# Kernel tuning notes

Hardware: AMD Instinct MI355X
Metric: run time of the kernel (lower is better)

## Reference

```python
import jax, jax.numpy as jnp
import numpy as np

BS, NQ, NH, HD = 4, 10000, 8, 32   # batch, queries, heads, head_dim
NP = 4                              # sampling points
H, W = 100, 100                     # fixed spatial shape (value_spatial_shapes_list[0])


def grid_sample_bilinear_zeros(img, grid):
    """PyTorch F.grid_sample(mode='bilinear', padding_mode='zeros', align_corners=False).
    img: (N, C, Hin, Win); grid: (N, Hg, Wg, 2) with (x, y) in [-1, 1].
    Returns (N, C, Hg, Wg)."""
    N, C, Hin, Win = img.shape
    Hg, Wg = grid.shape[1], grid.shape[2]
    # unnormalize (align_corners=False)
    x = (grid[..., 0] + 1.0) * (Win * 0.5) - 0.5
    y = (grid[..., 1] + 1.0) * (Hin * 0.5) - 0.5
    x0 = jnp.floor(x); y0 = jnp.floor(y)
    x1 = x0 + 1.0;     y1 = y0 + 1.0
    wx1 = x - x0; wx0 = 1.0 - wx1
    wy1 = y - y0; wy0 = 1.0 - wy1
    img_flat = img.reshape(N, C, Hin * Win)

    def gather(xi, yi, w):
        xi_i = xi.astype(jnp.int32); yi_i = yi.astype(jnp.int32)
        valid = (xi_i >= 0) & (xi_i < Win) & (yi_i >= 0) & (yi_i < Hin)
        xc = jnp.clip(xi_i, 0, Win - 1); yc = jnp.clip(yi_i, 0, Hin - 1)
        idx = (yc * Win + xc).reshape(N, 1, Hg * Wg)
        vals = jnp.take_along_axis(img_flat, idx, axis=2)      # (N, C, Hg*Wg)
        wm = jnp.where(valid, w, 0.0).reshape(N, 1, Hg * Wg)
        return vals * wm

    out = (gather(x0, y0, wx0 * wy0) + gather(x1, y0, wx1 * wy0)
           + gather(x0, y1, wx0 * wy1) + gather(x1, y1, wx1 * wy1))
    return out.reshape(N, C, Hg, Wg)


def setup_inputs() -> dict:
    key = jax.random.key(0)
    k1, k2, k3 = jax.random.split(key, 3)
    value = jax.random.normal(k1, (BS, H * W, NH, HD), dtype=jnp.float32)
    value_spatial_shapes = jnp.array([[H, W]], dtype=jnp.int64)  # unused (fixed-size variant)
    sampling_locations = jax.random.uniform(k2, (BS, NQ, NH, 1, NP, 2), dtype=jnp.float32)
    attention_weights = jax.random.uniform(k3, (BS, NQ, NH, 1, NP), dtype=jnp.float32)
    return {"value": value, "value_spatial_shapes": value_spatial_shapes,
            "sampling_locations": sampling_locations, "attention_weights": attention_weights}


def reference(value, value_spatial_shapes, sampling_locations, attention_weights):
    bs, _, nh, d = value.shape
    nq, npnt = sampling_locations.shape[1], sampling_locations.shape[4]
    # (bs, HW, nh, d) -> (bs*nh, d, H, W)
    v = jnp.transpose(value, (0, 2, 3, 1)).reshape(bs * nh, d, H, W)
    # sampling grids in [-1, 1]; single level -> index 0
    grids = 2.0 * sampling_locations[:, :, :, 0] - 1.0           # (bs, nq, nh, np, 2)
    grids = jnp.transpose(grids, (0, 2, 1, 3, 4)).reshape(bs * nh, nq, npnt, 2)
    sampled = grid_sample_bilinear_zeros(v, grids)               # (bs*nh, d, nq, np)
    aw = jnp.transpose(attention_weights, (0, 2, 1, 3, 4)).reshape(bs * nh, 1, nq, npnt)
    out = (sampled * aw).sum(-1)                                 # (bs*nh, d, nq)
    out = out.reshape(bs, nh * d, nq)
    return jnp.transpose(out, (0, 2, 1))                         # (bs, nq, nh*d)
```

## Files before the change

kernel.cpp:

```cpp
#include <hip/hip_runtime.h>


constexpr int BS = 4, NQ = 10000, NH = 8, HD = 32, NP = 4, H = 100, W = 100;
constexpr int HW = H * W;
constexpr int NGROUP = BS * NQ * NH;
constexpr int LANES_PER_GROUP = 8;

typedef float f32x4 __attribute__((ext_vector_type(4)));

__global__ __launch_bounds__(256)
void deform_attn_kernel(const float* __restrict__ value,
                        const float* __restrict__ sloc,
                        const float* __restrict__ aw,
                        float* __restrict__ out)
{
    const int tid   = blockIdx.x * 256 + threadIdx.x;
    const int group = tid >> 3;
    const int lane  = tid & 7;
    if (group >= NGROUP) return;

    const int h  = group & (NH - 1);
    const int bq = group >> 3;
    const int b  = bq / NQ;

    const f32x4 l01 = __builtin_nontemporal_load((const f32x4*)(sloc + (size_t)group * (NP * 2)));
    const f32x4 l23 = __builtin_nontemporal_load((const f32x4*)(sloc + (size_t)group * (NP * 2) + 4));
    const f32x4 wv  = __builtin_nontemporal_load((const f32x4*)(aw   + (size_t)group * NP));

    const float lx[NP] = {l01.x, l01.z, l23.x, l23.z};
    const float ly[NP] = {l01.y, l01.w, l23.y, l23.w};
    const float wp[NP] = {wv.x,  wv.y,  wv.z,  wv.w};

    const float* vbase = value + (size_t)b * HW * NH * HD + h * HD + lane * 4;

    f32x4 acc = (f32x4)(0.f);

#pragma unroll
    for (int p = 0; p < NP; ++p) {
        const float x = lx[p] * (float)W - 0.5f;
        const float y = ly[p] * (float)H - 0.5f;
        const float x0f = floorf(x);
        const float y0f = floorf(y);
        const int   x0  = (int)x0f, y0 = (int)y0f;
        const int   x1  = x0 + 1,   y1 = y0 + 1;
        const float wx1 = x - x0f,  wx0 = 1.f - wx1;
        const float wy1 = y - y0f,  wy0 = 1.f - wy1;

        const bool vx0 = (unsigned)x0 < (unsigned)W;
        const bool vx1 = (unsigned)x1 < (unsigned)W;
        const bool vy0 = (unsigned)y0 < (unsigned)H;
        const bool vy1 = (unsigned)y1 < (unsigned)H;

        const int xc0 = min(max(x0, 0), W - 1);
        const int xc1 = min(max(x1, 0), W - 1);
        const int yc0 = min(max(y0, 0), H - 1);
        const int yc1 = min(max(y1, 0), H - 1);

        const float w00 = (vx0 && vy0) ? wp[p] * wx0 * wy0 : 0.f;
        const float w10 = (vx1 && vy0) ? wp[p] * wx1 * wy0 : 0.f;
        const float w01 = (vx0 && vy1) ? wp[p] * wx0 * wy1 : 0.f;
        const float w11 = (vx1 && vy1) ? wp[p] * wx1 * wy1 : 0.f;

        const f32x4 v00 = *(const f32x4*)(vbase + (size_t)(yc0 * W + xc0) * (NH * HD));
        const f32x4 v10 = *(const f32x4*)(vbase + (size_t)(yc0 * W + xc1) * (NH * HD));
        const f32x4 v01 = *(const f32x4*)(vbase + (size_t)(yc1 * W + xc0) * (NH * HD));
        const f32x4 v11 = *(const f32x4*)(vbase + (size_t)(yc1 * W + xc1) * (NH * HD));

        acc += w00 * v00 + w10 * v10 + w01 * v01 + w11 * v11;
    }

    __builtin_nontemporal_store(acc, (f32x4*)(out + (size_t)bq * (NH * HD) + h * HD + lane * 4));
}

extern "C" void kernel_launch(void* const* d_in, const int* in_sizes, int n_in,
                              void* d_out, int out_size, void* d_ws, size_t ws_size,
                              hipStream_t stream) {
    const float* value = (const float*)d_in[0];
    const float* sloc  = (const float*)d_in[2];
    const float* aw    = (const float*)d_in[3];
    float*       out   = (float*)d_out;

    const int total_threads = NGROUP * LANES_PER_GROUP;
    const int block = 256;
    const int grid  = (total_threads + block - 1) / block;
    deform_attn_kernel<<<grid, block, 0, stream>>>(value, sloc, aw, out);
}
```

Before: 151.6 us.

## Remap blocks by batch/head-half and process two queries per thread

```diff
diff --git a/kernel.cpp b/kernel.cpp
--- a/kernel.cpp
+++ b/kernel.cpp
@@ -3,38 +3,15 @@
 
 constexpr int BS = 4, NQ = 10000, NH = 8, HD = 32, NP = 4, H = 100, W = 100;
 constexpr int HW = H * W;
-constexpr int NGROUP = BS * NQ * NH;
-constexpr int LANES_PER_GROUP = 8;
+constexpr int NQH = NQ / 2;
 
 typedef float f32x4 __attribute__((ext_vector_type(4)));
 
-__global__ __launch_bounds__(256)
-void deform_attn_kernel(const float* __restrict__ value,
-                        const float* __restrict__ sloc,
-                        const float* __restrict__ aw,
-                        float* __restrict__ out)
+__device__ __forceinline__ void bilinear_accum(const float lx[NP], const float ly[NP],
+                                               const float wp[NP],
+                                               const float* __restrict__ vbase,
+                                               f32x4& acc)
 {
-    const int tid   = blockIdx.x * 256 + threadIdx.x;
-    const int group = tid >> 3;
-    const int lane  = tid & 7;
-    if (group >= NGROUP) return;
-
-    const int h  = group & (NH - 1);
-    const int bq = group >> 3;
-    const int b  = bq / NQ;
-
-    const f32x4 l01 = __builtin_nontemporal_load((const f32x4*)(sloc + (size_t)group * (NP * 2)));
-    const f32x4 l23 = __builtin_nontemporal_load((const f32x4*)(sloc + (size_t)group * (NP * 2) + 4));
-    const f32x4 wv  = __builtin_nontemporal_load((const f32x4*)(aw   + (size_t)group * NP));
-
-    const float lx[NP] = {l01.x, l01.z, l23.x, l23.z};
-    const float ly[NP] = {l01.y, l01.w, l23.y, l23.w};
-    const float wp[NP] = {wv.x,  wv.y,  wv.z,  wv.w};
-
-    const float* vbase = value + (size_t)b * HW * NH * HD + h * HD + lane * 4;
-
-    f32x4 acc = (f32x4)(0.f);
-
 #pragma unroll
     for (int p = 0; p < NP; ++p) {
         const float x = lx[p] * (float)W - 0.5f;
@@ -68,8 +45,54 @@
 
         acc += w00 * v00 + w10 * v10 + w01 * v01 + w11 * v11;
     }
+}
 
-    __builtin_nontemporal_store(acc, (f32x4*)(out + (size_t)bq * (NH * HD) + h * HD + lane * 4));
+__global__ __launch_bounds__(256)
+void deform_attn_kernel(const float* __restrict__ value,
+                        const float* __restrict__ sloc,
+                        const float* __restrict__ aw,
+                        float* __restrict__ out)
+{
+    const int quad = blockIdx.x & 7;
+    const int c    = blockIdx.x >> 3;
+
+    const int t    = threadIdx.x;
+    const int lane = t & 7;
+    const int h_i  = (t >> 3) & 3;
+    const int slot = t >> 5;
+
+    const int b = quad >> 1;
+    const int h = ((quad & 1) << 2) + h_i;
+    const int q = (c << 3) + slot;
+
+    const int bq1 = b * NQ + q;
+    const int bq2 = bq1 + NQH;
+
+    const size_t p1 = (size_t)bq1 * NH + h;
+    const size_t p2 = (size_t)bq2 * NH + h;
+    const f32x4 a01 = *(const f32x4*)(sloc + p1 * (NP * 2));
+    const f32x4 a23 = *(const f32x4*)(sloc + p1 * (NP * 2) + 4);
+    const f32x4 awa = *(const f32x4*)(aw   + p1 * NP);
+    const f32x4 b01 = *(const f32x4*)(sloc + p2 * (NP * 2));
+    const f32x4 b23 = *(const f32x4*)(sloc + p2 * (NP * 2) + 4);
+    const f32x4 awb = *(const f32x4*)(aw   + p2 * NP);
+
+    const float lxa[NP] = {a01.x, a01.z, a23.x, a23.z};
+    const float lya[NP] = {a01.y, a01.w, a23.y, a23.w};
+    const float wpa[NP] = {awa.x, awa.y, awa.z, awa.w};
+    const float lxb[NP] = {b01.x, b01.z, b23.x, b23.z};
+    const float lyb[NP] = {b01.y, b01.w, b23.y, b23.w};
+    const float wpb[NP] = {awb.x, awb.y, awb.z, awb.w};
+
+    const float* vbase = value + (size_t)b * HW * NH * HD + h * HD + lane * 4;
+
+    f32x4 acc1 = (f32x4)(0.f);
+    f32x4 acc2 = (f32x4)(0.f);
+    bilinear_accum(lxa, lya, wpa, vbase, acc1);
+    bilinear_accum(lxb, lyb, wpb, vbase, acc2);
+
+    __builtin_nontemporal_store(acc1, (f32x4*)(out + (size_t)bq1 * (NH * HD) + h * HD + lane * 4));
+    __builtin_nontemporal_store(acc2, (f32x4*)(out + (size_t)bq2 * (NH * HD) + h * HD + lane * 4));
 }
 
 extern "C" void kernel_launch(void* const* d_in, const int* in_sizes, int n_in,
@@ -80,8 +103,5 @@
     const float* aw    = (const float*)d_in[3];
     float*       out   = (float*)d_out;
 
-    const int total_threads = NGROUP * LANES_PER_GROUP;
-    const int block = 256;
-    const int grid  = (total_threads + block - 1) / block;
-    deform_attn_kernel<<<grid, block, 0, stream>>>(value, sloc, aw, out);
+    deform_attn_kernel<<<5000, 256, 0, stream>>>(value, sloc, aw, out);
 }
```

Measured after the change: 135.9 us. 10.3% less time.
